# Kernel tuning notes

Hardware: AMD Instinct MI355X
Metric: run time of the kernel (lower is better)

Reference implementation:

```python
import jax, jax.numpy as jnp
import numpy as np

N = 512          # N_ROIs (nodes)
E = N * N        # number of edges
V = 6            # number of views (edge_attr dim)
DIMS = [(1, 36), (36, 24), (24, 5)]  # (in, out) per NNConv layer


def _nnconv(x, edge_attr, src, dst, We, be, root, bias, cin, cout):
    # edge MLP: Linear + ReLU -> per-edge weight matrix [E, cin, cout]
    w = jax.nn.relu(edge_attr @ We + be).reshape(-1, cin, cout)
    msg = jnp.einsum('ei,eio->eo', x[src], w)              # gather + per-edge matmul
    s = jax.ops.segment_sum(msg, dst, num_segments=N)      # scatter-sum
    cnt = jax.ops.segment_sum(jnp.ones((msg.shape[0], 1), x.dtype), dst, num_segments=N)
    agg = s / jnp.maximum(cnt, 1.0)                        # mean aggregation
    return agg + x @ root + bias                           # root weight + bias (PyG NNConv)


def setup_inputs() -> dict:
    key = jax.random.key(0)
    ks = jax.random.split(key, 16)
    x = jnp.ones((N, 1), jnp.float32)
    edge_attr = jax.random.uniform(ks[0], (E, V), jnp.float32)
    edge_index = jax.random.randint(ks[1], (2, E), 0, N, dtype=jnp.int32)
    inp = {'x': x, 'edge_attr': edge_attr, 'edge_index': edge_index}
    for l, (cin, cout) in enumerate(DIMS, start=1):
        k = jax.random.split(ks[1 + l], 4)
        inp[f'We{l}'] = jax.random.normal(k[0], (V, cin * cout), jnp.float32) / np.sqrt(V)
        inp[f'be{l}'] = jnp.zeros((cin * cout,), jnp.float32)
        inp[f'root{l}'] = jax.random.normal(k[1], (cin, cout), jnp.float32) / np.sqrt(cin)
        inp[f'b{l}'] = jnp.zeros((cout,), jnp.float32)
    return inp


def reference(x, edge_attr, edge_index,
              We1, be1, root1, b1,
              We2, be2, root2, b2,
              We3, be3, root3, b3):
    src, dst = edge_index[0], edge_index[1]
    h = jax.nn.relu(_nnconv(x, edge_attr, src, dst, We1, be1, root1, b1, *DIMS[0]))
    h = jax.nn.relu(_nnconv(h, edge_attr, src, dst, We2, be2, root2, b2, *DIMS[1]))
    h = jax.nn.relu(_nnconv(h, edge_attr, src, dst, We3, be3, root3, b3, *DIMS[2]))
    # pairwise CBT: sum_k |h_i,k - h_j,k|  ->  [N, N]
    cbt = jnp.sum(jnp.abs(h[:, None, :] - h[None, :, :]), axis=2)
    return cbt
```

## Files before the change

kernel.cpp:

```cpp
#include <hip/hip_runtime.h>
#include <hip/hip_bf16.h>

#define N_NODES 512
#define N_EDGES (512 * 512)
#define NBLK 256
#define EPB (N_EDGES / NBLK)

typedef __attribute__((ext_vector_type(2))) _Float16 half2v;

#if defined(__has_builtin)
#if __has_builtin(__builtin_amdgcn_fdot2)
#define FDOT2(a, b, c) __builtin_amdgcn_fdot2((a), (b), (c), false)
#endif
#endif
#ifndef FDOT2
static __device__ inline float fdot2_asm(half2v a, half2v b, float c) {
    float d;
    asm("v_dot2_f32_f16 %0, %1, %2, %3" : "=v"(d) : "v"(a), "v"(b), "v"(c));
    return d;
}
#define FDOT2(a, b, c) fdot2_asm((a), (b), (c))
#endif

static __device__ inline unsigned pack_h2(float x, float y) {
    union { _Float16 h[2]; unsigned u; } c;
    c.h[0] = (_Float16)x;
    c.h[1] = (_Float16)y;
    return c.u;
}
static __device__ inline half2v bits_h2(int b) {
    union { int i; half2v h; } c;
    c.i = b;
    return c.h;
}

__global__ __launch_bounds__(256) void count_kernel(const int* __restrict__ dst,
                                                    int* __restrict__ bcnt) {
    __shared__ int h[N_NODES];
    int tid = threadIdx.x;
    int b = blockIdx.x;
    h[tid] = 0;
    h[tid + 256] = 0;
    __syncthreads();
#pragma unroll
    for (int k = 0; k < EPB / 256; k++)
        atomicAdd(&h[dst[b * EPB + k * 256 + tid]], 1);
    __syncthreads();
    bcnt[b * N_NODES + tid] = h[tid];
    bcnt[b * N_NODES + tid + 256] = h[tid + 256];
}

__global__ __launch_bounds__(NBLK) void colscan_kernel(const int* __restrict__ bcnt,
                                                       int* __restrict__ pre,
                                                       int* __restrict__ tot) {
    __shared__ int buf[NBLK];
    int t = blockIdx.x;
    int b = threadIdx.x;
    int v = bcnt[b * N_NODES + t];
    buf[b] = v;
    __syncthreads();
    for (int d = 1; d < NBLK; d <<= 1) {
        int add = (b >= d) ? buf[b - d] : 0;
        __syncthreads();
        buf[b] += add;
        __syncthreads();
    }
    pre[b * N_NODES + t] = buf[b] - v;
    if (b == NBLK - 1) tot[t] = buf[b];
}

__global__ __launch_bounds__(512) void offs_kernel(const int* __restrict__ tot,
                                                   int* __restrict__ offs) {
    __shared__ int buf[N_NODES];
    int t = threadIdx.x;
    int v = tot[t];
    buf[t] = v;
    __syncthreads();
    for (int d = 1; d < N_NODES; d <<= 1) {
        int add = (t >= d) ? buf[t - d] : 0;
        __syncthreads();
        buf[t] += add;
        __syncthreads();
    }
    offs[t + 1] = buf[t];
    if (t == 0) offs[0] = 0;
}

__global__ __launch_bounds__(256) void scatter_kernel(const int* __restrict__ src,
                                                      const int* __restrict__ dst,
                                                      const float* __restrict__ ea,
                                                      const int* __restrict__ pre,
                                                      const int* __restrict__ offs,
                                                      int4* __restrict__ ed4) {
    __shared__ int lcur[N_NODES];
    int tid = threadIdx.x;
    int b = blockIdx.x;
    lcur[tid] = offs[tid] + pre[b * N_NODES + tid];
    lcur[tid + 256] = offs[tid + 256] + pre[b * N_NODES + tid + 256];
    __syncthreads();
#pragma unroll
    for (int k = 0; k < EPB / 256; k++) {
        int e = b * EPB + k * 256 + tid;
        const float* a = ea + (size_t)e * 6;
        float a0 = a[0], a1 = a[1], a2 = a[2], a3 = a[3], a4 = a[4], a5 = a[5];
        int p = atomicAdd(&lcur[dst[e]], 1);
        int4 r;
        r.x = (int)pack_h2(a0, a1);
        r.y = (int)pack_h2(a2, a3);
        r.z = (int)pack_h2(a4, a5);
        r.w = src[e];
        ed4[p] = r;
    }
}

template <int CIN, int COUT, int OG, int BLK, int G>
__global__ __launch_bounds__(BLK) void nnconv_edges(
    const float* __restrict__ hprev,
    const int4* __restrict__ ed4,
    const int* __restrict__ offs,
    const float* __restrict__ We,
    const float* __restrict__ be,
    float* __restrict__ agg)
{
    constexpr int J = CIN * COUT;
    constexpr int OPL = COUT / OG;
    constexpr int A = CIN * OPL;

    const int n = blockIdx.x / G;
    const int g = blockIdx.x % G;
    const int tid = threadIdx.x;
    const bool act = (tid < A);
    const int i = act ? tid / OPL : 0;
    const int og = act ? (tid % OPL) * OG : 0;

    half2v wrp[OG][3];
    float ber[OG], acc[OG];
#pragma unroll
    for (int k = 0; k < OG; k++) {
        acc[k] = 0.f;
        int j = i * COUT + og + k;
        if (act) {
            ber[k] = be[j];
#pragma unroll
            for (int t = 0; t < 3; t++)
                wrp[k][t] = bits_h2((int)pack_h2(We[(2 * t) * J + j], We[(2 * t + 1) * J + j]));
        } else {
            ber[k] = 0.f;
#pragma unroll
            for (int t = 0; t < 3; t++) wrp[k][t] = bits_h2(0);
        }
    }

    const int start = offs[n];
    const int end = offs[n + 1];
    const int len = end - start;
    const int per = (len + G - 1) / G;
    int p = start + g * per;
    int p1 = p + per;
    if (p1 > end) p1 = end;

    auto proc4 = [&](const int4* ed) {
        float xv[4];
#pragma unroll
        for (int u = 0; u < 4; u++)
            xv[u] = hprev[(ed[u].w & (N_NODES - 1)) * CIN + i];
#pragma unroll
        for (int u = 0; u < 4; u++) {
            half2v e01 = bits_h2(ed[u].x), e23 = bits_h2(ed[u].y), e45 = bits_h2(ed[u].z);
#pragma unroll
            for (int k = 0; k < OG; k++) {
                float z = FDOT2(e45, wrp[k][2],
                        FDOT2(e23, wrp[k][1],
                        FDOT2(e01, wrp[k][0], ber[k])));
                acc[k] = fmaf(xv[u], fmaxf(z, 0.f), acc[k]);
            }
        }
    };

    const int nb = (p1 - p) >> 2;
    {
        const int4* ep = ed4 + p;
        int4 bufA[4], bufB[4];
        if (nb > 0) {
#pragma unroll
            for (int u = 0; u < 4; u++) bufA[u] = ep[u];
            int b = 0;
            while (b + 2 <= nb) {
#pragma unroll
                for (int u = 0; u < 4; u++) bufB[u] = ep[4 + u];
                proc4(bufA);
                ep += 4; ++b;
                if (b + 2 <= nb) {
#pragma unroll
                    for (int u = 0; u < 4; u++) bufA[u] = ep[4 + u];
                    proc4(bufB);
                    ep += 4; ++b;
                } else {
                    proc4(bufB);
                    ep += 4; ++b;
                }
            }
            if (b < nb) proc4(bufA);
        }
    }
    for (int q = p + (nb << 2); q < p1; ++q) {
        int4 ed = ed4[q];
        float xv = hprev[(ed.w & (N_NODES - 1)) * CIN + i];
        half2v e01 = bits_h2(ed.x), e23 = bits_h2(ed.y), e45 = bits_h2(ed.z);
#pragma unroll
        for (int k = 0; k < OG; k++) {
            float z = FDOT2(e45, wrp[k][2],
                    FDOT2(e23, wrp[k][1],
                    FDOT2(e01, wrp[k][0], ber[k])));
            acc[k] = fmaf(xv, fmaxf(z, 0.f), acc[k]);
        }
    }

    if constexpr (CIN == 1) {
        if (act) atomicAdd(&agg[n * COUT + og], acc[0]);
    } else {
        __shared__ float lds_acc[J];
        if (act) {
#pragma unroll
            for (int k = 0; k < OG; k++) lds_acc[i * COUT + og + k] = acc[k];
        }
        __syncthreads();
        if (tid < COUT) {
            float sum = 0.f;
#pragma unroll
            for (int ii = 0; ii < CIN; ii++) sum += lds_acc[ii * COUT + tid];
            atomicAdd(&agg[n * COUT + tid], sum);
        }
    }
}

template <int CIN, int COUT>
__global__ __launch_bounds__(64) void nnconv_fin(const float* __restrict__ agg,
                                                 const int* __restrict__ offs,
                                                 const float* __restrict__ hprev,
                                                 const float* __restrict__ root,
                                                 const float* __restrict__ bias,
                                                 float* __restrict__ hout) {
    int n = blockIdx.x;
    int t = threadIdx.x;
    if (t >= COUT) return;
    int cnt = offs[n + 1] - offs[n];
    float inv = 1.f / fmaxf((float)cnt, 1.f);
    float v = agg[n * COUT + t] * inv;
#pragma unroll
    for (int i = 0; i < CIN; i++) v = fmaf(hprev[n * CIN + i], root[i * COUT + t], v);
    v += bias[t];
    hout[n * COUT + t] = fmaxf(v, 0.f);
}

__global__ __launch_bounds__(256) void cbt_kernel(const float* __restrict__ h3,
                                                  float* __restrict__ out) {
    __shared__ float lh[N_NODES * 5];
    int tid = threadIdx.x;
    for (int idx = tid; idx < N_NODES * 5; idx += 256) lh[idx] = h3[idx];
    __syncthreads();
    int i = blockIdx.x;
    float hi[5];
#pragma unroll
    for (int k = 0; k < 5; k++) hi[k] = lh[i * 5 + k];
    for (int j = tid; j < N_NODES; j += 256) {
        float sacc = 0.f;
#pragma unroll
        for (int k = 0; k < 5; k++) sacc += fabsf(hi[k] - lh[j * 5 + k]);
        out[i * N_NODES + j] = sacc;
    }
}

extern "C" void kernel_launch(void* const* d_in, const int* in_sizes, int n_in,
                              void* d_out, int out_size, void* d_ws, size_t ws_size,
                              hipStream_t stream) {
    const float* x = (const float*)d_in[0];
    const float* edge_attr = (const float*)d_in[1];
    const int* edge_index = (const int*)d_in[2];
    const float* We1 = (const float*)d_in[3];
    const float* be1 = (const float*)d_in[4];
    const float* root1 = (const float*)d_in[5];
    const float* b1 = (const float*)d_in[6];
    const float* We2 = (const float*)d_in[7];
    const float* be2 = (const float*)d_in[8];
    const float* root2 = (const float*)d_in[9];
    const float* b2 = (const float*)d_in[10];
    const float* We3 = (const float*)d_in[11];
    const float* be3 = (const float*)d_in[12];
    const float* root3 = (const float*)d_in[13];
    const float* b3 = (const float*)d_in[14];

    const int E = N_EDGES;
    const int* src = edge_index;
    const int* dst = edge_index + E;

    char* ws = (char*)d_ws;
    int* offs = (int*)(ws + 0);
    int* bcnt = (int*)(ws + 4096);
    int* pre = (int*)(ws + 528384);
    int4* ed4 = (int4*)(ws + 1052672);
    int* tot = (int*)(ws + 1052672);
    float* agg1 = (float*)(ws + 5246976);
    float* agg2 = (float*)(ws + 5320704);
    float* agg3 = (float*)(ws + 5369856);
    float* h1 = (float*)(ws + 5380096);
    float* h2 = (float*)(ws + 5453824);
    float* h3 = (float*)(ws + 5502976);

    hipMemsetAsync(agg1, 0, 5380096 - 5246976, stream);

    count_kernel<<<NBLK, 256, 0, stream>>>(dst, bcnt);
    colscan_kernel<<<N_NODES, NBLK, 0, stream>>>(bcnt, pre, tot);
    offs_kernel<<<1, 512, 0, stream>>>(tot, offs);
    scatter_kernel<<<NBLK, 256, 0, stream>>>(src, dst, edge_attr, pre, offs, ed4);

    nnconv_edges<1, 36, 1, 64, 16><<<N_NODES * 16, 64, 0, stream>>>(x, ed4, offs, We1, be1, agg1);
    nnconv_fin<1, 36><<<N_NODES, 64, 0, stream>>>(agg1, offs, x, root1, b1, h1);

    nnconv_edges<36, 24, 4, 256, 8><<<N_NODES * 8, 256, 0, stream>>>(h1, ed4, offs, We2, be2, agg2);
    nnconv_fin<36, 24><<<N_NODES, 64, 0, stream>>>(agg2, offs, h1, root2, b2, h2);

    nnconv_edges<24, 5, 1, 128, 8><<<N_NODES * 8, 128, 0, stream>>>(h2, ed4, offs, We3, be3, agg3);
    nnconv_fin<24, 5><<<N_NODES, 64, 0, stream>>>(agg3, offs, h2, root3, b3, h3);

    cbt_kernel<<<N_NODES, 256, 0, stream>>>(h3, (float*)d_out);
}
```

Baseline: 197.0 us.

## Stage edge chunks in LDS and split edges across thread groups

Each edge-conv block now loads 256 edge records cooperatively into shared memory, prefetching the next chunk into registers, instead of every thread streaming the same records from global memory. Threads are divided into SPLIT groups that each handle a strided subset of edges, and their partial sums are combined with LDS atomics. Grid and block sizes are retuned for all three layers. The block-count histogram is also stored transposed so the column scan reads contiguously. This trades redundant global loads for extra barriers and LDS traffic.

Result: slower. 205.9 us (+4.5%).

```diff
diff --git a/kernel.cpp b/kernel.cpp
--- a/kernel.cpp
+++ b/kernel.cpp
@@ -35,7 +35,7 @@
 }
 
 __global__ __launch_bounds__(256) void count_kernel(const int* __restrict__ dst,
-                                                    int* __restrict__ bcnt) {
+                                                    int* __restrict__ bcnt_t) {
     __shared__ int h[N_NODES];
     int tid = threadIdx.x;
     int b = blockIdx.x;
@@ -46,17 +46,17 @@
     for (int k = 0; k < EPB / 256; k++)
         atomicAdd(&h[dst[b * EPB + k * 256 + tid]], 1);
     __syncthreads();
-    bcnt[b * N_NODES + tid] = h[tid];
-    bcnt[b * N_NODES + tid + 256] = h[tid + 256];
-}
-
-__global__ __launch_bounds__(NBLK) void colscan_kernel(const int* __restrict__ bcnt,
+    bcnt_t[tid * NBLK + b] = h[tid];
+    bcnt_t[(tid + 256) * NBLK + b] = h[tid + 256];
+}
+
+__global__ __launch_bounds__(NBLK) void colscan_kernel(const int* __restrict__ bcnt_t,
                                                        int* __restrict__ pre,
                                                        int* __restrict__ tot) {
     __shared__ int buf[NBLK];
     int t = blockIdx.x;
     int b = threadIdx.x;
-    int v = bcnt[b * N_NODES + t];
+    int v = bcnt_t[t * NBLK + b];
     buf[b] = v;
     __syncthreads();
     for (int d = 1; d < NBLK; d <<= 1) {
@@ -113,7 +113,7 @@
     }
 }
 
-template <int CIN, int COUT, int OG, int BLK, int G>
+template <int CIN, int COUT, int OG, int BLK, int G, int SPLIT>
 __global__ __launch_bounds__(BLK) void nnconv_edges(
     const float* __restrict__ hprev,
     const int4* __restrict__ ed4,
@@ -125,13 +125,20 @@
     constexpr int J = CIN * COUT;
     constexpr int OPL = COUT / OG;
     constexpr int A = CIN * OPL;
+    constexpr int GRP = BLK / SPLIT;
+    constexpr int CH = 256;
+
+    __shared__ int4 ebuf[CH];
+    __shared__ float lds_acc[J];
 
     const int n = blockIdx.x / G;
     const int g = blockIdx.x % G;
     const int tid = threadIdx.x;
-    const bool act = (tid < A);
-    const int i = act ? tid / OPL : 0;
-    const int og = act ? (tid % OPL) * OG : 0;
+    const int t = tid & (GRP - 1);
+    const int s = tid / GRP;
+    const bool act = (t < A);
+    const int i = act ? t / OPL : 0;
+    const int og = act ? (t % OPL) * OG : 0;
 
     half2v wrp[OG][3];
     float ber[OG], acc[OG];
@@ -142,12 +149,12 @@
         if (act) {
             ber[k] = be[j];
 #pragma unroll
-            for (int t = 0; t < 3; t++)
-                wrp[k][t] = bits_h2((int)pack_h2(We[(2 * t) * J + j], We[(2 * t + 1) * J + j]));
+            for (int tt = 0; tt < 3; tt++)
+                wrp[k][tt] = bits_h2((int)pack_h2(We[(2 * tt) * J + j], We[(2 * tt + 1) * J + j]));
         } else {
             ber[k] = 0.f;
 #pragma unroll
-            for (int t = 0; t < 3; t++) wrp[k][t] = bits_h2(0);
+            for (int tt = 0; tt < 3; tt++) wrp[k][tt] = bits_h2(0);
         }
     }
 
@@ -155,82 +162,79 @@
     const int end = offs[n + 1];
     const int len = end - start;
     const int per = (len + G - 1) / G;
-    int p = start + g * per;
-    int p1 = p + per;
+    int p0 = start + g * per;
+    int p1 = p0 + per;
+    if (p0 > end) p0 = end;
     if (p1 > end) p1 = end;
 
-    auto proc4 = [&](const int4* ed) {
-        float xv[4];
-#pragma unroll
-        for (int u = 0; u < 4; u++)
-            xv[u] = hprev[(ed[u].w & (N_NODES - 1)) * CIN + i];
-#pragma unroll
-        for (int u = 0; u < 4; u++) {
-            half2v e01 = bits_h2(ed[u].x), e23 = bits_h2(ed[u].y), e45 = bits_h2(ed[u].z);
-#pragma unroll
-            for (int k = 0; k < OG; k++) {
-                float z = FDOT2(e45, wrp[k][2],
-                        FDOT2(e23, wrp[k][1],
-                        FDOT2(e01, wrp[k][0], ber[k])));
-                acc[k] = fmaf(xv[u], fmaxf(z, 0.f), acc[k]);
+    const float* hp_i = hprev + i;
+
+    int p = p0;
+    int4 st;
+    {
+        int c0 = p1 - p0;
+        if (c0 > CH) c0 = CH;
+        if (tid < c0) st = ed4[p0 + tid];
+    }
+    while (p < p1) {
+        int cnt = p1 - p;
+        if (cnt > CH) cnt = CH;
+        if (tid < cnt) ebuf[tid] = st;
+        __syncthreads();
+        int np = p + cnt;
+        if (np < p1) {
+            int nc = p1 - np;
+            if (nc > CH) nc = CH;
+            if (tid < nc) st = ed4[np + tid];
+        }
+        int k = s;
+        for (; k + 7 * SPLIT < cnt; k += 8 * SPLIT) {
+            int4 e[8];
+            float xg[8];
+#pragma unroll
+            for (int u = 0; u < 8; u++) e[u] = ebuf[k + u * SPLIT];
+#pragma unroll
+            for (int u = 0; u < 8; u++) xg[u] = hp_i[(e[u].w & (N_NODES - 1)) * CIN];
+#pragma unroll
+            for (int u = 0; u < 8; u++) {
+                half2v e01 = bits_h2(e[u].x), e23 = bits_h2(e[u].y), e45 = bits_h2(e[u].z);
+#pragma unroll
+                for (int kk = 0; kk < OG; kk++) {
+                    float z = FDOT2(e45, wrp[kk][2],
+                            FDOT2(e23, wrp[kk][1],
+                            FDOT2(e01, wrp[kk][0], ber[kk])));
+                    acc[kk] = fmaf(xg[u], fmaxf(z, 0.f), acc[kk]);
+                }
             }
         }
-    };
-
-    const int nb = (p1 - p) >> 2;
-    {
-        const int4* ep = ed4 + p;
-        int4 bufA[4], bufB[4];
-        if (nb > 0) {
-#pragma unroll
-            for (int u = 0; u < 4; u++) bufA[u] = ep[u];
-            int b = 0;
-            while (b + 2 <= nb) {
-#pragma unroll
-                for (int u = 0; u < 4; u++) bufB[u] = ep[4 + u];
-                proc4(bufA);
-                ep += 4; ++b;
-                if (b + 2 <= nb) {
-#pragma unroll
-                    for (int u = 0; u < 4; u++) bufA[u] = ep[4 + u];
-                    proc4(bufB);
-                    ep += 4; ++b;
-                } else {
-                    proc4(bufB);
-                    ep += 4; ++b;
-                }
+        for (; k < cnt; k += SPLIT) {
+            int4 e = ebuf[k];
+            float xv = hp_i[(e.w & (N_NODES - 1)) * CIN];
+            half2v e01 = bits_h2(e.x), e23 = bits_h2(e.y), e45 = bits_h2(e.z);
+#pragma unroll
+            for (int kk = 0; kk < OG; kk++) {
+                float z = FDOT2(e45, wrp[kk][2],
+                        FDOT2(e23, wrp[kk][1],
+                        FDOT2(e01, wrp[kk][0], ber[kk])));
+                acc[kk] = fmaf(xv, fmaxf(z, 0.f), acc[kk]);
             }
-            if (b < nb) proc4(bufA);
         }
-    }
-    for (int q = p + (nb << 2); q < p1; ++q) {
-        int4 ed = ed4[q];
-        float xv = hprev[(ed.w & (N_NODES - 1)) * CIN + i];
-        half2v e01 = bits_h2(ed.x), e23 = bits_h2(ed.y), e45 = bits_h2(ed.z);
-#pragma unroll
-        for (int k = 0; k < OG; k++) {
-            float z = FDOT2(e45, wrp[k][2],
-                    FDOT2(e23, wrp[k][1],
-                    FDOT2(e01, wrp[k][0], ber[k])));
-            acc[k] = fmaf(xv, fmaxf(z, 0.f), acc[k]);
-        }
-    }
-
-    if constexpr (CIN == 1) {
-        if (act) atomicAdd(&agg[n * COUT + og], acc[0]);
-    } else {
-        __shared__ float lds_acc[J];
-        if (act) {
-#pragma unroll
-            for (int k = 0; k < OG; k++) lds_acc[i * COUT + og + k] = acc[k];
-        }
-        __syncthreads();
-        if (tid < COUT) {
-            float sum = 0.f;
-#pragma unroll
-            for (int ii = 0; ii < CIN; ii++) sum += lds_acc[ii * COUT + tid];
-            atomicAdd(&agg[n * COUT + tid], sum);
-        }
+        __syncthreads();
+        p = np;
+    }
+
+    for (int j = tid; j < J; j += BLK) lds_acc[j] = 0.f;
+    __syncthreads();
+    if (act) {
+#pragma unroll
+        for (int kk = 0; kk < OG; kk++) atomicAdd(&lds_acc[i * COUT + og + kk], acc[kk]);
+    }
+    __syncthreads();
+    if (tid < COUT) {
+        float sum = 0.f;
+#pragma unroll
+        for (int ii = 0; ii < CIN; ii++) sum += lds_acc[ii * COUT + tid];
+        atomicAdd(&agg[n * COUT + tid], sum);
     }
 }
 
@@ -296,10 +300,10 @@
 
     char* ws = (char*)d_ws;
     int* offs = (int*)(ws + 0);
-    int* bcnt = (int*)(ws + 4096);
+    int* tot = (int*)(ws + 2048);
+    int* bcnt_t = (int*)(ws + 4096);
     int* pre = (int*)(ws + 528384);
     int4* ed4 = (int4*)(ws + 1052672);
-    int* tot = (int*)(ws + 1052672);
     float* agg1 = (float*)(ws + 5246976);
     float* agg2 = (float*)(ws + 5320704);
     float* agg3 = (float*)(ws + 5369856);
@@ -309,18 +313,18 @@
 
     hipMemsetAsync(agg1, 0, 5380096 - 5246976, stream);
 
-    count_kernel<<<NBLK, 256, 0, stream>>>(dst, bcnt);
-    colscan_kernel<<<N_NODES, NBLK, 0, stream>>>(bcnt, pre, tot);
+    count_kernel<<<NBLK, 256, 0, stream>>>(dst, bcnt_t);
+    colscan_kernel<<<N_NODES, NBLK, 0, stream>>>(bcnt_t, pre, tot);
     offs_kernel<<<1, 512, 0, stream>>>(tot, offs);
     scatter_kernel<<<NBLK, 256, 0, stream>>>(src, dst, edge_attr, pre, offs, ed4);
 
-    nnconv_edges<1, 36, 1, 64, 16><<<N_NODES * 16, 64, 0, stream>>>(x, ed4, offs, We1, be1, agg1);
+    nnconv_edges<1, 36, 1, 256, 4, 4><<<N_NODES * 4, 256, 0, stream>>>(x, ed4, offs, We1, be1, agg1);
     nnconv_fin<1, 36><<<N_NODES, 64, 0, stream>>>(agg1, offs, x, root1, b1, h1);
 
-    nnconv_edges<36, 24, 4, 256, 8><<<N_NODES * 8, 256, 0, stream>>>(h1, ed4, offs, We2, be2, agg2);
+    nnconv_edges<36, 24, 4, 256, 4, 1><<<N_NODES * 4, 256, 0, stream>>>(h1, ed4, offs, We2, be2, agg2);
     nnconv_fin<36, 24><<<N_NODES, 64, 0, stream>>>(agg2, offs, h1, root2, b2, h2);
 
-    nnconv_edges<24, 5, 1, 128, 8><<<N_NODES * 8, 128, 0, stream>>>(h2, ed4, offs, We3, be3, agg3);
+    nnconv_edges<24, 5, 1, 256, 4, 2><<<N_NODES * 4, 256, 0, stream>>>(h2, ed4, offs, We3, be3, agg3);
     nnconv_fin<24, 5><<<N_NODES, 64, 0, stream>>>(agg3, offs, h2, root3, b3, h3);
 
     cbt_kernel<<<N_NODES, 256, 0, stream>>>(h3, (float*)d_out);
```

## Fuse NNConv finalize into edge kernel via last-block counter and drop memset

Applied to the files above, without the earlier changes.

Removes the separate nnconv_fin launches: each edge block bumps a per-node done counter and the last block for a node applies mean, root weight, bias and ReLU. The agg memset is folded into count_kernel, and the done counters are zeroed in colscan by reusing rows of a now-transposed bcnt buffer so colscan reads coalesced. The edge loop becomes a simple 8-wide batch with a masked tail, and layer 2 switches to OG=8 with 128 threads. This saves launches and one memset at the cost of threadfences and extra atomics, and it depends on reusing buffer rows once the scan has consumed them.

Measured after the change: 683.8 us. 3.47x slower.

```diff
diff --git a/kernel.cpp b/kernel.cpp
--- a/kernel.cpp
+++ b/kernel.cpp
@@ -35,28 +35,32 @@
 }
 
 __global__ __launch_bounds__(256) void count_kernel(const int* __restrict__ dst,
-                                                    int* __restrict__ bcnt) {
+                                                    int* __restrict__ bcnt_t,
+                                                    float* __restrict__ aggz) {
     __shared__ int h[N_NODES];
     int tid = threadIdx.x;
     int b = blockIdx.x;
     h[tid] = 0;
     h[tid + 256] = 0;
+    int gt = b * 256 + tid;
+    if (gt < 512 * (36 + 24 + 5)) aggz[gt] = 0.f;
     __syncthreads();
 #pragma unroll
     for (int k = 0; k < EPB / 256; k++)
         atomicAdd(&h[dst[b * EPB + k * 256 + tid]], 1);
     __syncthreads();
-    bcnt[b * N_NODES + tid] = h[tid];
-    bcnt[b * N_NODES + tid + 256] = h[tid + 256];
-}
-
-__global__ __launch_bounds__(NBLK) void colscan_kernel(const int* __restrict__ bcnt,
+    bcnt_t[tid * NBLK + b] = h[tid];
+    bcnt_t[(tid + 256) * NBLK + b] = h[tid + 256];
+}
+
+__global__ __launch_bounds__(NBLK) void colscan_kernel(const int* __restrict__ bcnt_t,
                                                        int* __restrict__ pre,
-                                                       int* __restrict__ tot) {
+                                                       int* __restrict__ tot,
+                                                       int* __restrict__ bz) {
     __shared__ int buf[NBLK];
     int t = blockIdx.x;
     int b = threadIdx.x;
-    int v = bcnt[b * N_NODES + t];
+    int v = bcnt_t[t * NBLK + b];
     buf[b] = v;
     __syncthreads();
     for (int d = 1; d < NBLK; d <<= 1) {
@@ -67,6 +71,7 @@
     }
     pre[b * N_NODES + t] = buf[b] - v;
     if (b == NBLK - 1) tot[t] = buf[b];
+    if (t >= N_NODES - 6) bz[t * NBLK + b] = 0;
 }
 
 __global__ __launch_bounds__(512) void offs_kernel(const int* __restrict__ tot,
@@ -120,11 +125,18 @@
     const int* __restrict__ offs,
     const float* __restrict__ We,
     const float* __restrict__ be,
-    float* __restrict__ agg)
+    const float* __restrict__ root,
+    const float* __restrict__ bias,
+    float* __restrict__ agg,
+    int* __restrict__ done,
+    float* __restrict__ hout)
 {
     constexpr int J = CIN * COUT;
     constexpr int OPL = COUT / OG;
     constexpr int A = CIN * OPL;
+
+    __shared__ float lds_acc[J];
+    __shared__ int lastf;
 
     const int n = blockIdx.x / G;
     const int g = blockIdx.x % G;
@@ -157,69 +169,55 @@
     const int per = (len + G - 1) / G;
     int p = start + g * per;
     int p1 = p + per;
+    if (p > end) p = end;
     if (p1 > end) p1 = end;
 
-    auto proc4 = [&](const int4* ed) {
-        float xv[4];
-#pragma unroll
-        for (int u = 0; u < 4; u++)
-            xv[u] = hprev[(ed[u].w & (N_NODES - 1)) * CIN + i];
-#pragma unroll
-        for (int u = 0; u < 4; u++) {
-            half2v e01 = bits_h2(ed[u].x), e23 = bits_h2(ed[u].y), e45 = bits_h2(ed[u].z);
+    const float* hp_i = hprev + i;
+
+    for (; p + 8 <= p1; p += 8) {
+        int4 e[8];
+#pragma unroll
+        for (int u = 0; u < 8; u++) e[u] = ed4[p + u];
+        float xg[8];
+#pragma unroll
+        for (int u = 0; u < 8; u++) xg[u] = hp_i[(e[u].w & (N_NODES - 1)) * CIN];
+#pragma unroll
+        for (int u = 0; u < 8; u++) {
+            half2v e01 = bits_h2(e[u].x), e23 = bits_h2(e[u].y), e45 = bits_h2(e[u].z);
 #pragma unroll
             for (int k = 0; k < OG; k++) {
                 float z = FDOT2(e45, wrp[k][2],
                         FDOT2(e23, wrp[k][1],
                         FDOT2(e01, wrp[k][0], ber[k])));
-                acc[k] = fmaf(xv[u], fmaxf(z, 0.f), acc[k]);
+                acc[k] = fmaf(xg[u], fmaxf(z, 0.f), acc[k]);
             }
         }
-    };
-
-    const int nb = (p1 - p) >> 2;
-    {
-        const int4* ep = ed4 + p;
-        int4 bufA[4], bufB[4];
-        if (nb > 0) {
-#pragma unroll
-            for (int u = 0; u < 4; u++) bufA[u] = ep[u];
-            int b = 0;
-            while (b + 2 <= nb) {
-#pragma unroll
-                for (int u = 0; u < 4; u++) bufB[u] = ep[4 + u];
-                proc4(bufA);
-                ep += 4; ++b;
-                if (b + 2 <= nb) {
-#pragma unroll
-                    for (int u = 0; u < 4; u++) bufA[u] = ep[4 + u];
-                    proc4(bufB);
-                    ep += 4; ++b;
-                } else {
-                    proc4(bufB);
-                    ep += 4; ++b;
-                }
+    }
+    if (p < p1) {
+        int4 e[8];
+        float xg[8];
+#pragma unroll
+        for (int u = 0; u < 8; u++)
+            e[u] = (p + u < p1) ? ed4[p + u] : make_int4(0, 0, 0, 0);
+#pragma unroll
+        for (int u = 0; u < 8; u++)
+            xg[u] = (p + u < p1) ? hp_i[(e[u].w & (N_NODES - 1)) * CIN] : 0.f;
+#pragma unroll
+        for (int u = 0; u < 8; u++) {
+            half2v e01 = bits_h2(e[u].x), e23 = bits_h2(e[u].y), e45 = bits_h2(e[u].z);
+#pragma unroll
+            for (int k = 0; k < OG; k++) {
+                float z = FDOT2(e45, wrp[k][2],
+                        FDOT2(e23, wrp[k][1],
+                        FDOT2(e01, wrp[k][0], ber[k])));
+                acc[k] = fmaf(xg[u], fmaxf(z, 0.f), acc[k]);
             }
-            if (b < nb) proc4(bufA);
-        }
-    }
-    for (int q = p + (nb << 2); q < p1; ++q) {
-        int4 ed = ed4[q];
-        float xv = hprev[(ed.w & (N_NODES - 1)) * CIN + i];
-        half2v e01 = bits_h2(ed.x), e23 = bits_h2(ed.y), e45 = bits_h2(ed.z);
-#pragma unroll
-        for (int k = 0; k < OG; k++) {
-            float z = FDOT2(e45, wrp[k][2],
-                    FDOT2(e23, wrp[k][1],
-                    FDOT2(e01, wrp[k][0], ber[k])));
-            acc[k] = fmaf(xv, fmaxf(z, 0.f), acc[k]);
         }
     }
 
     if constexpr (CIN == 1) {
         if (act) atomicAdd(&agg[n * COUT + og], acc[0]);
     } else {
-        __shared__ float lds_acc[J];
         if (act) {
 #pragma unroll
             for (int k = 0; k < OG; k++) lds_acc[i * COUT + og + k] = acc[k];
@@ -232,25 +230,22 @@
             atomicAdd(&agg[n * COUT + tid], sum);
         }
     }
-}
-
-template <int CIN, int COUT>
-__global__ __launch_bounds__(64) void nnconv_fin(const float* __restrict__ agg,
-                                                 const int* __restrict__ offs,
-                                                 const float* __restrict__ hprev,
-                                                 const float* __restrict__ root,
-                                                 const float* __restrict__ bias,
-                                                 float* __restrict__ hout) {
-    int n = blockIdx.x;
-    int t = threadIdx.x;
-    if (t >= COUT) return;
-    int cnt = offs[n + 1] - offs[n];
-    float inv = 1.f / fmaxf((float)cnt, 1.f);
-    float v = agg[n * COUT + t] * inv;
-#pragma unroll
-    for (int i = 0; i < CIN; i++) v = fmaf(hprev[n * CIN + i], root[i * COUT + t], v);
-    v += bias[t];
-    hout[n * COUT + t] = fmaxf(v, 0.f);
+
+    __threadfence();
+    if (tid == 0) lastf = (atomicAdd(&done[n], 1) == G - 1) ? 1 : 0;
+    __syncthreads();
+    if (lastf) {
+        __threadfence();
+        if (tid < COUT) {
+            float inv = 1.f / fmaxf((float)len, 1.f);
+            float v = agg[n * COUT + tid] * inv;
+#pragma unroll
+            for (int ii = 0; ii < CIN; ii++)
+                v = fmaf(hprev[n * CIN + ii], root[ii * COUT + tid], v);
+            v += bias[tid];
+            hout[n * COUT + tid] = fmaxf(v, 0.f);
+        }
+    }
 }
 
 __global__ __launch_bounds__(256) void cbt_kernel(const float* __restrict__ h3,
@@ -296,10 +291,10 @@
 
     char* ws = (char*)d_ws;
     int* offs = (int*)(ws + 0);
-    int* bcnt = (int*)(ws + 4096);
+    int* tot = (int*)(ws + 2048);
+    int* bcnt_t = (int*)(ws + 4096);
     int* pre = (int*)(ws + 528384);
     int4* ed4 = (int4*)(ws + 1052672);
-    int* tot = (int*)(ws + 1052672);
     float* agg1 = (float*)(ws + 5246976);
     float* agg2 = (float*)(ws + 5320704);
     float* agg3 = (float*)(ws + 5369856);
@@ -307,21 +302,23 @@
     float* h2 = (float*)(ws + 5453824);
     float* h3 = (float*)(ws + 5502976);
 
-    hipMemsetAsync(agg1, 0, 5380096 - 5246976, stream);
-
-    count_kernel<<<NBLK, 256, 0, stream>>>(dst, bcnt);
-    colscan_kernel<<<N_NODES, NBLK, 0, stream>>>(bcnt, pre, tot);
+    int* done1 = bcnt_t + 506 * NBLK;
+    int* done2 = bcnt_t + 508 * NBLK;
+    int* done3 = bcnt_t + 510 * NBLK;
+
+    count_kernel<<<NBLK, 256, 0, stream>>>(dst, bcnt_t, agg1 );
+    colscan_kernel<<<N_NODES, NBLK, 0, stream>>>(bcnt_t, pre, tot, bcnt_t);
     offs_kernel<<<1, 512, 0, stream>>>(tot, offs);
     scatter_kernel<<<NBLK, 256, 0, stream>>>(src, dst, edge_attr, pre, offs, ed4);
 
-    nnconv_edges<1, 36, 1, 64, 16><<<N_NODES * 16, 64, 0, stream>>>(x, ed4, offs, We1, be1, agg1);
-    nnconv_fin<1, 36><<<N_NODES, 64, 0, stream>>>(agg1, offs, x, root1, b1, h1);
-
-    nnconv_edges<36, 24, 4, 256, 8><<<N_NODES * 8, 256, 0, stream>>>(h1, ed4, offs, We2, be2, agg2);
-    nnconv_fin<36, 24><<<N_NODES, 64, 0, stream>>>(agg2, offs, h1, root2, b2, h2);
-
-    nnconv_edges<24, 5, 1, 128, 8><<<N_NODES * 8, 128, 0, stream>>>(h2, ed4, offs, We3, be3, agg3);
-    nnconv_fin<24, 5><<<N_NODES, 64, 0, stream>>>(agg3, offs, h2, root3, b3, h3);
+    nnconv_edges<1, 36, 1, 64, 16><<<N_NODES * 16, 64, 0, stream>>>(
+        x, ed4, offs, We1, be1, root1, b1, agg1, done1, h1);
+
+    nnconv_edges<36, 24, 8, 128, 8><<<N_NODES * 8, 128, 0, stream>>>(
+        h1, ed4, offs, We2, be2, root2, b2, agg2, done2, h2);
+
+    nnconv_edges<24, 5, 1, 128, 8><<<N_NODES * 8, 128, 0, stream>>>(
+        h2, ed4, offs, We3, be3, root3, b3, agg3, done3, h3);
 
     cbt_kernel<<<N_NODES, 256, 0, stream>>>(h3, (float*)d_out);
 }
```
